# Kernel tuning notes

Measured on AMD Instinct MI355X. Metric: run time of the kernel, lower is better.

## Reference

```python
import jax, jax.numpy as jnp
import numpy as np

N_NODES = 50000


def sage_conv(x, edge_index, w_l, w_r, b):
    # PyG SAGEConv (aggr='mean', root_weight=True):
    #   out = mean_{j in N(i)} x_j @ w_l + x_i @ w_r + b
    src = edge_index[0]  # message source j
    dst = edge_index[1]  # message target i
    msgs = x[src]                                        # [E, C_in] gather
    agg = jax.ops.segment_sum(msgs, dst, num_segments=N_NODES)   # [N, C_in]
    deg = jax.ops.segment_sum(jnp.ones((src.shape[0],), x.dtype), dst,
                              num_segments=N_NODES)              # [N]
    agg = agg / jnp.maximum(deg, 1.0)[:, None]           # mean aggregation
    return agg @ w_l + x @ w_r + b


def setup_inputs() -> dict:
    key = jax.random.key(0)
    ks = jax.random.split(key, 8)
    in_c, hid_c, out_c = 96, 128, 64
    x = jax.random.normal(ks[0], (N_NODES, in_c), dtype=jnp.float32)
    edge_index = jax.random.randint(ks[1], (2, 800000), 0, N_NODES, dtype=jnp.int64)
    def glorot(k, fan_in, fan_out):
        lim = float(np.sqrt(6.0 / (fan_in + fan_out)))
        return jax.random.uniform(k, (fan_in, fan_out), jnp.float32, -lim, lim)
    return {
        'x': x,
        'edge_index': edge_index,
        'w1_l': glorot(ks[2], in_c, hid_c),
        'w1_r': glorot(ks[3], in_c, hid_c),
        'b1': jnp.zeros((hid_c,), jnp.float32),
        'w2_l': glorot(ks[4], hid_c, out_c),
        'w2_r': glorot(ks[5], hid_c, out_c),
        'b2': jnp.zeros((out_c,), jnp.float32),
    }


def reference(x, edge_index, w1_l, w1_r, b1, w2_l, w2_r, b2):
    h = sage_conv(x, edge_index, w1_l, w1_r, b1)
    h = jax.nn.relu(h)
    out = sage_conv(h, edge_index, w2_l, w2_r, b2)
    return out
```

## Files before the change

kernel.cpp:

```cpp
#include <hip/hip_runtime.h>
#include <hip/hip_bf16.h>

#define N_NODES 50000
#define IN_C    96
#define HID_C   128
#define OUT_C   64
#define MROWS   50048

#define NB      200
#define BSZ     250
#define WCHUNK  4096
#define NWG     196
#define BCAP    8192

#define XBLKS   2344
#define WBLKS   160

typedef __attribute__((ext_vector_type(8))) short short8;
typedef __attribute__((ext_vector_type(4))) float f32x4;

__device__ inline unsigned int f2bf(float f) {
    unsigned int u = __float_as_uint(f);
    return (u + 0x7fffu + ((u >> 16) & 1u)) >> 16;
}
__device__ inline unsigned int pack2(float lo, float hi) {
    return f2bf(lo) | (f2bf(hi) << 16);
}
__device__ inline float blo(unsigned int u) { return __uint_as_float(u << 16); }
__device__ inline float bhi(unsigned int u) { return __uint_as_float(u & 0xffff0000u); }

__global__ __launch_bounds__(256) void conv_all_kernel(
    const float* __restrict__ x, uint4* __restrict__ xb4,
    const float* __restrict__ w1l, const float* __restrict__ w1r,
    const float* __restrict__ w2l, const float* __restrict__ w2r,
    unsigned short* __restrict__ wt1, unsigned short* __restrict__ wt2,
    int* __restrict__ gcnt)
{
    int blk = blockIdx.x;
    if (blk == gridDim.x - 1 && threadIdx.x < NB) gcnt[threadIdx.x] = 0;
    if (blk < XBLKS) {
        int idx = blk * 256 + threadIdx.x;
        if (idx >= N_NODES * 12) return;
        const float4* x4 = (const float4*)x;
        float4 u = x4[(size_t)idx * 2];
        float4 v = x4[(size_t)idx * 2 + 1];
        uint4 w;
        w.x = pack2(u.x, u.y); w.y = pack2(u.z, u.w);
        w.z = pack2(v.x, v.y); w.w = pack2(v.z, v.w);
        xb4[idx] = w;
    } else {
        int i = (blk - XBLKS) * 256 + threadIdx.x;
        if (i < 128 * 192) {
            int col = i / 192, k = i - col * 192;
            float v = (k < 96) ? w1l[k * 128 + col] : w1r[(k - 96) * 128 + col];
            wt1[i] = (unsigned short)f2bf(v);
        } else {
            int j = i - 128 * 192;
            int col = j / 128, k = j - col * 128;
            float v = (col < 64) ? w2l[k * 64 + col] : w2r[k * 64 + col - 64];
            wt2[j] = (unsigned short)f2bf(v);
        }
    }
}

__global__ __launch_bounds__(256) void csr_scatter(
    const int* __restrict__ src, const int* __restrict__ dst,
    int* __restrict__ gcnt, unsigned int* __restrict__ pairs, int E)
{
    __shared__ int lsrc[WCHUNK];
    __shared__ int ldst[WCHUNK];
    __shared__ int h[NB];
    __shared__ int wbase[NB];
    int t = threadIdx.x;
    int base_e = blockIdx.x * WCHUNK;
    int rem = E - base_e; if (rem > WCHUNK) rem = WCHUNK;
    {
        const int4* s4 = (const int4*)(src + base_e);
        const int4* d4 = (const int4*)(dst + base_e);
        int nv = rem >> 2;
        for (int k = t; k < nv; k += 256) {
            ((int4*)lsrc)[k] = s4[k];
            ((int4*)ldst)[k] = d4[k];
        }
        for (int i = (nv << 2) + t; i < rem; i += 256) {
            lsrc[i] = src[base_e + i];
            ldst[i] = dst[base_e + i];
        }
    }
    if (t < NB) h[t] = 0;
    __syncthreads();
    for (int i = t; i < rem; i += 256)
        atomicAdd(&h[ldst[i] / BSZ], 1);
    __syncthreads();
    if (t < NB) {
        wbase[t] = atomicAdd(&gcnt[t], h[t]);
        h[t] = 0;
    }
    __syncthreads();
    for (int i = t; i < rem; i += 256) {
        int d = ldst[i];
        int b = d / BSZ;
        int r = atomicAdd(&h[b], 1);
        pairs[b * BCAP + wbase[b] + r] =
            ((unsigned)(d - b * BSZ) << 17) | (unsigned)lsrc[i];
    }
}

__global__ __launch_bounds__(256) void partb_csr(
    const unsigned int* __restrict__ pairs, const int* __restrict__ gcnt,
    int* __restrict__ rowstart, int* __restrict__ cnt,
    int* __restrict__ adj)
{
    __shared__ int h[256];
    __shared__ int buf[256];
    __shared__ int cur[256];
    int b = blockIdx.x;
    int t = threadIdx.x;
    int beg = b * BCAP;
    int n = gcnt[b];
    int node0 = b * BSZ;
    h[t] = 0;
    __syncthreads();
    const uint4* p4 = (const uint4*)(pairs + beg);
    int nv = n >> 2;
    for (int k = t; k < nv; k += 256) {
        uint4 u = p4[k];
        atomicAdd(&h[u.x >> 17], 1);
        atomicAdd(&h[u.y >> 17], 1);
        atomicAdd(&h[u.z >> 17], 1);
        atomicAdd(&h[u.w >> 17], 1);
    }
    for (int i = (nv << 2) + t; i < n; i += 256)
        atomicAdd(&h[pairs[beg + i] >> 17], 1);
    __syncthreads();
    int c = h[t];
    buf[t] = c;
    __syncthreads();
    for (int off = 1; off < 256; off <<= 1) {
        int v = (t >= off) ? buf[t - off] : 0;
        __syncthreads();
        buf[t] += v;
        __syncthreads();
    }
    int excl = buf[t] - c;
    if (t < BSZ) {
        rowstart[node0 + t] = beg + excl;
        cnt[node0 + t] = c;
    }
    cur[t] = beg + excl;
    __syncthreads();
    for (int k = t; k < nv; k += 256) {
        uint4 u = p4[k];
        int p0 = atomicAdd(&cur[u.x >> 17], 1);
        int p1 = atomicAdd(&cur[u.y >> 17], 1);
        int p2 = atomicAdd(&cur[u.z >> 17], 1);
        int p3 = atomicAdd(&cur[u.w >> 17], 1);
        adj[p0] = (int)(u.x & 0x1FFFFu);
        adj[p1] = (int)(u.y & 0x1FFFFu);
        adj[p2] = (int)(u.z & 0x1FFFFu);
        adj[p3] = (int)(u.w & 0x1FFFFu);
    }
    for (int i = (nv << 2) + t; i < n; i += 256) {
        unsigned int u = pairs[beg + i];
        int pos = atomicAdd(&cur[u >> 17], 1);
        adj[pos] = (int)(u & 0x1FFFFu);
    }
}

__global__ __launch_bounds__(256) void gather1_kernel(
    const int* __restrict__ rowstart, const int* __restrict__ cnt,
    const int* __restrict__ adj, const uint4* __restrict__ xb4,
    uint4* __restrict__ agg4)
{
    int idx = blockIdx.x * 256 + threadIdx.x;
    if (idx >= N_NODES * 12) return;
    int node = idx / 12;
    int c = idx - node * 12;
    int beg = rowstart[node];
    int d = cnt[node];
    int end = beg + d;
    float a0=0,a1=0,a2=0,a3=0,a4=0,a5=0,a6=0,a7=0;
    float b0=0,b1=0,b2=0,b3=0,b4=0,b5=0,b6=0,b7=0;
    int j = beg;
    for (; j + 3 < end; j += 4) {
        int s0 = adj[j];
        int s1 = adj[j + 1];
        int s2 = adj[j + 2];
        int s3 = adj[j + 3];
        uint4 u = xb4[(size_t)s0 * 12 + c];
        uint4 v = xb4[(size_t)s1 * 12 + c];
        uint4 w = xb4[(size_t)s2 * 12 + c];
        uint4 z = xb4[(size_t)s3 * 12 + c];
        a0 += blo(u.x); a1 += bhi(u.x); a2 += blo(u.y); a3 += bhi(u.y);
        a4 += blo(u.z); a5 += bhi(u.z); a6 += blo(u.w); a7 += bhi(u.w);
        b0 += blo(v.x); b1 += bhi(v.x); b2 += blo(v.y); b3 += bhi(v.y);
        b4 += blo(v.z); b5 += bhi(v.z); b6 += blo(v.w); b7 += bhi(v.w);
        a0 += blo(w.x); a1 += bhi(w.x); a2 += blo(w.y); a3 += bhi(w.y);
        a4 += blo(w.z); a5 += bhi(w.z); a6 += blo(w.w); a7 += bhi(w.w);
        b0 += blo(z.x); b1 += bhi(z.x); b2 += blo(z.y); b3 += bhi(z.y);
        b4 += blo(z.z); b5 += bhi(z.z); b6 += blo(z.w); b7 += bhi(z.w);
    }
    for (; j < end; j++) {
        int s0 = adj[j];
        uint4 u = xb4[(size_t)s0 * 12 + c];
        a0 += blo(u.x); a1 += bhi(u.x); a2 += blo(u.y); a3 += bhi(u.y);
        a4 += blo(u.z); a5 += bhi(u.z); a6 += blo(u.w); a7 += bhi(u.w);
    }
    a0 += b0; a1 += b1; a2 += b2; a3 += b3;
    a4 += b4; a5 += b5; a6 += b6; a7 += b7;
    float id = 1.0f / (float)max(d, 1);
    uint4 w;
    w.x = pack2(a0 * id, a1 * id); w.y = pack2(a2 * id, a3 * id);
    w.z = pack2(a4 * id, a5 * id); w.w = pack2(a6 * id, a7 * id);
    agg4[(size_t)node * 12 + c] = w;
}

__global__ __launch_bounds__(256) void gemm12_fused(
    const uint4* __restrict__ agg4, const uint4* __restrict__ xb4,
    const uint4* __restrict__ w1t4, const uint4* __restrict__ w2t4,
    const float* __restrict__ b1, const float* __restrict__ b2,
    unsigned short* __restrict__ p, float* __restrict__ out)
{
    constexpr int KP = 200;
    constexpr int KQ = 136;
    __shared__ unsigned short la[64 * KP];
    int t = threadIdx.x;
    uint4* la4 = (uint4*)la;

    int wave = t >> 6, lane = t & 63;
    int m = lane & 15, half = lane >> 4;
    int koff = half * 8;

    const short8* w1s = (const short8*)w1t4;
    short8 B1r[6][2];
#pragma unroll
    for (int kk = 0; kk < 6; kk++) {
        B1r[kk][0] = w1s[(wave * 32 + m)      * 24 + kk * 4 + half];
        B1r[kk][1] = w1s[(wave * 32 + 16 + m) * 24 + kk * 4 + half];
    }

    int row0 = blockIdx.x * 64;
    for (int i = t; i < 64 * 24; i += 256) {
        int r = i / 24, c = i - r * 24;
        la4[r * 25 + c] = (c < 12)
            ? agg4[(size_t)(row0 + r) * 12 + c]
            : xb4[(size_t)(row0 + r) * 12 + (c - 12)];
    }
    __syncthreads();

    f32x4 acc[4][2] = {};
#pragma unroll
    for (int kk = 0; kk < 6; kk++) {
        int k0 = kk * 32;
#pragma unroll
        for (int g = 0; g < 4; g++) {
            short8 A = *(const short8*)&la[(g * 16 + m) * KP + k0 + koff];
            acc[g][0] = __builtin_amdgcn_mfma_f32_16x16x32_bf16(A, B1r[kk][0], acc[g][0], 0, 0, 0);
            acc[g][1] = __builtin_amdgcn_mfma_f32_16x16x32_bf16(A, B1r[kk][1], acc[g][1], 0, 0, 0);
        }
    }
    __syncthreads();

    const short8* w2s = (const short8*)w2t4;
    short8 B2r[4][2];
#pragma unroll
    for (int kk = 0; kk < 4; kk++) {
        B2r[kk][0] = w2s[(wave * 32 + m)      * 16 + kk * 4 + half];
        B2r[kk][1] = w2s[(wave * 32 + 16 + m) * 16 + kk * 4 + half];
    }

    int col0 = wave * 32 + m, col1 = col0 + 16;
    {
        float bias0 = b1[col0], bias1 = b1[col1];
#pragma unroll
        for (int g = 0; g < 4; g++) {
#pragma unroll
            for (int reg = 0; reg < 4; reg++) {
                int hr = g * 16 + half * 4 + reg;
                la[hr * KQ + col0] = (unsigned short)f2bf(fmaxf(acc[g][0][reg] + bias0, 0.f));
                la[hr * KQ + col1] = (unsigned short)f2bf(fmaxf(acc[g][1][reg] + bias1, 0.f));
            }
        }
    }
    __syncthreads();

    f32x4 acc2[4][2] = {};
#pragma unroll
    for (int kk = 0; kk < 4; kk++) {
        int k0 = kk * 32;
#pragma unroll
        for (int g = 0; g < 4; g++) {
            short8 A = *(const short8*)&la[(g * 16 + m) * KQ + k0 + koff];
            acc2[g][0] = __builtin_amdgcn_mfma_f32_16x16x32_bf16(A, B2r[kk][0], acc2[g][0], 0, 0, 0);
            acc2[g][1] = __builtin_amdgcn_mfma_f32_16x16x32_bf16(A, B2r[kk][1], acc2[g][1], 0, 0, 0);
        }
    }
#pragma unroll
    for (int g = 0; g < 4; g++) {
#pragma unroll
        for (int reg = 0; reg < 4; reg++) {
            int r = row0 + g * 16 + half * 4 + reg;
            if (r >= N_NODES) continue;
            float v0 = acc2[g][0][reg], v1 = acc2[g][1][reg];
            if (col0 < 64) p[(size_t)r * 64 + col0] = (unsigned short)f2bf(v0);
            else           out[(size_t)r * 64 + col0 - 64] = v0 + b2[col0 - 64];
            if (col1 < 64) p[(size_t)r * 64 + col1] = (unsigned short)f2bf(v1);
            else           out[(size_t)r * 64 + col1 - 64] = v1 + b2[col1 - 64];
        }
    }
}

__global__ __launch_bounds__(256) void gather2_kernel(
    const int* __restrict__ rowstart, const int* __restrict__ cnt,
    const int* __restrict__ adj, const uint4* __restrict__ p4,
    float* __restrict__ out)
{
    int idx = blockIdx.x * 256 + threadIdx.x;
    if (idx >= N_NODES * 8) return;
    int node = idx >> 3;
    int c = idx & 7;
    int beg = rowstart[node];
    int d = cnt[node];
    int end = beg + d;
    float a0=0,a1=0,a2=0,a3=0,a4=0,a5=0,a6=0,a7=0;
    float b0=0,b1=0,b2=0,b3=0,b4=0,b5=0,b6=0,b7=0;
    int j = beg;
    for (; j + 3 < end; j += 4) {
        int s0 = adj[j];
        int s1 = adj[j + 1];
        int s2 = adj[j + 2];
        int s3 = adj[j + 3];
        uint4 u = p4[(size_t)s0 * 8 + c];
        uint4 v = p4[(size_t)s1 * 8 + c];
        uint4 w = p4[(size_t)s2 * 8 + c];
        uint4 z = p4[(size_t)s3 * 8 + c];
        a0 += blo(u.x); a1 += bhi(u.x); a2 += blo(u.y); a3 += bhi(u.y);
        a4 += blo(u.z); a5 += bhi(u.z); a6 += blo(u.w); a7 += bhi(u.w);
        b0 += blo(v.x); b1 += bhi(v.x); b2 += blo(v.y); b3 += bhi(v.y);
        b4 += blo(v.z); b5 += bhi(v.z); b6 += blo(v.w); b7 += bhi(v.w);
        a0 += blo(w.x); a1 += bhi(w.x); a2 += blo(w.y); a3 += bhi(w.y);
        a4 += blo(w.z); a5 += bhi(w.z); a6 += blo(w.w); a7 += bhi(w.w);
        b0 += blo(z.x); b1 += bhi(z.x); b2 += blo(z.y); b3 += bhi(z.y);
        b4 += blo(z.z); b5 += bhi(z.z); b6 += blo(z.w); b7 += bhi(z.w);
    }
    for (; j < end; j++) {
        int s0 = adj[j];
        uint4 u = p4[(size_t)s0 * 8 + c];
        a0 += blo(u.x); a1 += bhi(u.x); a2 += blo(u.y); a3 += bhi(u.y);
        a4 += blo(u.z); a5 += bhi(u.z); a6 += blo(u.w); a7 += bhi(u.w);
    }
    a0 += b0; a1 += b1; a2 += b2; a3 += b3;
    a4 += b4; a5 += b5; a6 += b6; a7 += b7;
    float id = 1.0f / (float)max(d, 1);
    float4* o4 = (float4*)out;
    size_t base = (size_t)node * 16 + 2 * c;
    float4 u = o4[base], v = o4[base + 1];
    u.x = fmaf(a0, id, u.x); u.y = fmaf(a1, id, u.y);
    u.z = fmaf(a2, id, u.z); u.w = fmaf(a3, id, u.w);
    v.x = fmaf(a4, id, v.x); v.y = fmaf(a5, id, v.y);
    v.z = fmaf(a6, id, v.z); v.w = fmaf(a7, id, v.w);
    o4[base] = u; o4[base + 1] = v;
}

extern "C" void kernel_launch(void* const* d_in, const int* in_sizes, int n_in,
                              void* d_out, int out_size, void* d_ws, size_t ws_size,
                              hipStream_t stream)
{
    const float* x   = (const float*)d_in[0];
    const int*   ei  = (const int*)d_in[1];
    const float* w1l = (const float*)d_in[2];
    const float* w1r = (const float*)d_in[3];
    const float* b1  = (const float*)d_in[4];
    const float* w2l = (const float*)d_in[5];
    const float* w2r = (const float*)d_in[6];
    const float* b2  = (const float*)d_in[7];
    float* out = (float*)d_out;

    int E = in_sizes[1] / 2;
    const int* src = ei;
    const int* dst = ei + E;

    int* gcnt     = (int*)d_ws;
    int* cnt      = gcnt + 256;
    int* rowstart = cnt + N_NODES;
    unsigned int* pairs = (unsigned int*)(rowstart + N_NODES);
    int* adj      = (int*)(pairs + NB * BCAP);
    unsigned short* xb  = (unsigned short*)(adj + NB * BCAP);
    unsigned short* agg = xb + (size_t)MROWS * IN_C;
    unsigned short* p   = agg + (size_t)MROWS * IN_C;
    unsigned short* Wt1 = p  + (size_t)N_NODES * 64;
    unsigned short* Wt2 = Wt1 + 128 * 192;

    conv_all_kernel<<<XBLKS + WBLKS, 256, 0, stream>>>(
        x, (uint4*)xb, w1l, w1r, w2l, w2r, Wt1, Wt2, gcnt);

    csr_scatter<<<NWG, 256, 0, stream>>>(src, dst, gcnt, pairs, E);
    partb_csr<<<NB, 256, 0, stream>>>(pairs, gcnt, rowstart, cnt, adj);

    gather1_kernel<<<(N_NODES * 12 + 255) / 256, 256, 0, stream>>>(
        rowstart, cnt, adj, (const uint4*)xb, (uint4*)agg);

    gemm12_fused<<<MROWS / 64, 256, 0, stream>>>(
        (const uint4*)agg, (const uint4*)xb, (const uint4*)Wt1, (const uint4*)Wt2,
        b1, b2, p, out);

    gather2_kernel<<<(N_NODES * 8 + 255) / 256, 256, 0, stream>>>(
        rowstart, cnt, adj, (const uint4*)p, out);
}
```

Measured before the change: 163.0 us.

## Fuse layer-1 neighbor mean gather into the GEMM kernel via shared memory

Removes the separate gather1 kernel and computes each tile's mean-aggregated neighbor features directly into LDS inside the layer-1 GEMM kernel. This eliminates the round trip of the bf16 agg buffer through global memory and one kernel launch. In exchange, the latency-bound random gathers now run inside GEMM blocks with fewer concurrent threads per row, which may reduce latency hiding.

```diff
diff --git a/kernel.cpp b/kernel.cpp
--- a/kernel.cpp
+++ b/kernel.cpp
@@ -167,56 +167,9 @@
     }
 }
 
-__global__ __launch_bounds__(256) void gather1_kernel(
+__global__ __launch_bounds__(256) void gemm12_gather(
     const int* __restrict__ rowstart, const int* __restrict__ cnt,
     const int* __restrict__ adj, const uint4* __restrict__ xb4,
-    uint4* __restrict__ agg4)
-{
-    int idx = blockIdx.x * 256 + threadIdx.x;
-    if (idx >= N_NODES * 12) return;
-    int node = idx / 12;
-    int c = idx - node * 12;
-    int beg = rowstart[node];
-    int d = cnt[node];
-    int end = beg + d;
-    float a0=0,a1=0,a2=0,a3=0,a4=0,a5=0,a6=0,a7=0;
-    float b0=0,b1=0,b2=0,b3=0,b4=0,b5=0,b6=0,b7=0;
-    int j = beg;
-    for (; j + 3 < end; j += 4) {
-        int s0 = adj[j];
-        int s1 = adj[j + 1];
-        int s2 = adj[j + 2];
-        int s3 = adj[j + 3];
-        uint4 u = xb4[(size_t)s0 * 12 + c];
-        uint4 v = xb4[(size_t)s1 * 12 + c];
-        uint4 w = xb4[(size_t)s2 * 12 + c];
-        uint4 z = xb4[(size_t)s3 * 12 + c];
-        a0 += blo(u.x); a1 += bhi(u.x); a2 += blo(u.y); a3 += bhi(u.y);
-        a4 += blo(u.z); a5 += bhi(u.z); a6 += blo(u.w); a7 += bhi(u.w);
-        b0 += blo(v.x); b1 += bhi(v.x); b2 += blo(v.y); b3 += bhi(v.y);
-        b4 += blo(v.z); b5 += bhi(v.z); b6 += blo(v.w); b7 += bhi(v.w);
-        a0 += blo(w.x); a1 += bhi(w.x); a2 += blo(w.y); a3 += bhi(w.y);
-        a4 += blo(w.z); a5 += bhi(w.z); a6 += blo(w.w); a7 += bhi(w.w);
-        b0 += blo(z.x); b1 += bhi(z.x); b2 += blo(z.y); b3 += bhi(z.y);
-        b4 += blo(z.z); b5 += bhi(z.z); b6 += blo(z.w); b7 += bhi(z.w);
-    }
-    for (; j < end; j++) {
-        int s0 = adj[j];
-        uint4 u = xb4[(size_t)s0 * 12 + c];
-        a0 += blo(u.x); a1 += bhi(u.x); a2 += blo(u.y); a3 += bhi(u.y);
-        a4 += blo(u.z); a5 += bhi(u.z); a6 += blo(u.w); a7 += bhi(u.w);
-    }
-    a0 += b0; a1 += b1; a2 += b2; a3 += b3;
-    a4 += b4; a5 += b5; a6 += b6; a7 += b7;
-    float id = 1.0f / (float)max(d, 1);
-    uint4 w;
-    w.x = pack2(a0 * id, a1 * id); w.y = pack2(a2 * id, a3 * id);
-    w.z = pack2(a4 * id, a5 * id); w.w = pack2(a6 * id, a7 * id);
-    agg4[(size_t)node * 12 + c] = w;
-}
-
-__global__ __launch_bounds__(256) void gemm12_fused(
-    const uint4* __restrict__ agg4, const uint4* __restrict__ xb4,
     const uint4* __restrict__ w1t4, const uint4* __restrict__ w2t4,
     const float* __restrict__ b1, const float* __restrict__ b2,
     unsigned short* __restrict__ p, float* __restrict__ out)
@@ -226,6 +179,54 @@
     __shared__ unsigned short la[64 * KP];
     int t = threadIdx.x;
     uint4* la4 = (uint4*)la;
+    int row0 = blockIdx.x * 64;
+
+    for (int i = t; i < 64 * 12; i += 256) {
+        int r = i / 12, c = i - r * 12;
+        la4[r * 25 + 12 + c] = xb4[(size_t)(row0 + r) * 12 + c];
+    }
+
+    for (int u = t; u < 64 * 12; u += 256) {
+        int r = u / 12, c = u - r * 12;
+        int node = row0 + r;
+        if (node >= N_NODES) continue;
+        int beg = rowstart[node];
+        int d = cnt[node];
+        int end = beg + d;
+        float a0=0,a1=0,a2=0,a3=0,a4=0,a5=0,a6=0,a7=0;
+        float b0=0,b1_=0,b2_=0,b3=0,b4=0,b5=0,b6=0,b7=0;
+        int j = beg;
+        for (; j + 3 < end; j += 4) {
+            int s0 = adj[j];
+            int s1 = adj[j + 1];
+            int s2 = adj[j + 2];
+            int s3 = adj[j + 3];
+            uint4 uu = xb4[(size_t)s0 * 12 + c];
+            uint4 vv = xb4[(size_t)s1 * 12 + c];
+            uint4 ww = xb4[(size_t)s2 * 12 + c];
+            uint4 zz = xb4[(size_t)s3 * 12 + c];
+            a0 += blo(uu.x); a1 += bhi(uu.x); a2 += blo(uu.y); a3 += bhi(uu.y);
+            a4 += blo(uu.z); a5 += bhi(uu.z); a6 += blo(uu.w); a7 += bhi(uu.w);
+            b0 += blo(vv.x); b1_ += bhi(vv.x); b2_ += blo(vv.y); b3 += bhi(vv.y);
+            b4 += blo(vv.z); b5 += bhi(vv.z); b6 += blo(vv.w); b7 += bhi(vv.w);
+            a0 += blo(ww.x); a1 += bhi(ww.x); a2 += blo(ww.y); a3 += bhi(ww.y);
+            a4 += blo(ww.z); a5 += bhi(ww.z); a6 += blo(ww.w); a7 += bhi(ww.w);
+            b0 += blo(zz.x); b1_ += bhi(zz.x); b2_ += blo(zz.y); b3 += bhi(zz.y);
+            b4 += blo(zz.z); b5 += bhi(zz.z); b6 += blo(zz.w); b7 += bhi(zz.w);
+        }
+        for (; j < end; j++) {
+            uint4 uu = xb4[(size_t)adj[j] * 12 + c];
+            a0 += blo(uu.x); a1 += bhi(uu.x); a2 += blo(uu.y); a3 += bhi(uu.y);
+            a4 += blo(uu.z); a5 += bhi(uu.z); a6 += blo(uu.w); a7 += bhi(uu.w);
+        }
+        a0 += b0; a1 += b1_; a2 += b2_; a3 += b3;
+        a4 += b4; a5 += b5; a6 += b6; a7 += b7;
+        float id = 1.0f / (float)max(d, 1);
+        uint4 w;
+        w.x = pack2(a0 * id, a1 * id); w.y = pack2(a2 * id, a3 * id);
+        w.z = pack2(a4 * id, a5 * id); w.w = pack2(a6 * id, a7 * id);
+        la4[r * 25 + c] = w;
+    }
 
     int wave = t >> 6, lane = t & 63;
     int m = lane & 15, half = lane >> 4;
@@ -237,14 +238,6 @@
     for (int kk = 0; kk < 6; kk++) {
         B1r[kk][0] = w1s[(wave * 32 + m)      * 24 + kk * 4 + half];
         B1r[kk][1] = w1s[(wave * 32 + 16 + m) * 24 + kk * 4 + half];
-    }
-
-    int row0 = blockIdx.x * 64;
-    for (int i = t; i < 64 * 24; i += 256) {
-        int r = i / 24, c = i - r * 24;
-        la4[r * 25 + c] = (c < 12)
-            ? agg4[(size_t)(row0 + r) * 12 + c]
-            : xb4[(size_t)(row0 + r) * 12 + (c - 12)];
     }
     __syncthreads();
 
@@ -386,8 +379,7 @@
     unsigned int* pairs = (unsigned int*)(rowstart + N_NODES);
     int* adj      = (int*)(pairs + NB * BCAP);
     unsigned short* xb  = (unsigned short*)(adj + NB * BCAP);
-    unsigned short* agg = xb + (size_t)MROWS * IN_C;
-    unsigned short* p   = agg + (size_t)MROWS * IN_C;
+    unsigned short* p   = xb + (size_t)MROWS * IN_C;
     unsigned short* Wt1 = p  + (size_t)N_NODES * 64;
     unsigned short* Wt2 = Wt1 + 128 * 192;
 
@@ -397,12 +389,9 @@
     csr_scatter<<<NWG, 256, 0, stream>>>(src, dst, gcnt, pairs, E);
     partb_csr<<<NB, 256, 0, stream>>>(pairs, gcnt, rowstart, cnt, adj);
 
-    gather1_kernel<<<(N_NODES * 12 + 255) / 256, 256, 0, stream>>>(
-        rowstart, cnt, adj, (const uint4*)xb, (uint4*)agg);
-
-    gemm12_fused<<<MROWS / 64, 256, 0, stream>>>(
-        (const uint4*)agg, (const uint4*)xb, (const uint4*)Wt1, (const uint4*)Wt2,
-        b1, b2, p, out);
+    gemm12_gather<<<MROWS / 64, 256, 0, stream>>>(
+        rowstart, cnt, adj, (const uint4*)xb,
+        (const uint4*)Wt1, (const uint4*)Wt2, b1, b2, p, out);
 
     gather2_kernel<<<(N_NODES * 8 + 255) / 256, 256, 0, stream>>>(
         rowstart, cnt, adj, (const uint4*)p, out);
```

Result: slower. 177.7 us (+9.0%).
